# Kernel tuning notes

Measured on AMD Instinct MI355X. Metric: run time of the kernel, lower is better.

Reference implementation:

```python
import jax, jax.numpy as jnp
import numpy as np


def _gcn_conv(x, src, dst, W, b, n_nodes):
    # PyG GCNConv: add self-loops, symmetric deg^{-1/2} normalization, then linear.
    xw = x @ W  # [N, H]
    # degree including self-loop (count of incoming edges at dst + 1)
    deg = jnp.zeros((n_nodes,), dtype=xw.dtype).at[dst].add(1.0) + 1.0
    dinv = jax.lax.rsqrt(deg)  # deg >= 1 always
    coef = (dinv[src] * dinv[dst])[:, None]  # [E, 1]
    out = jnp.zeros_like(xw).at[dst].add(xw[src] * coef)
    # self-loop edge i->i has norm dinv[i]^2
    out = out + xw * (dinv * dinv)[:, None]
    return out + b


def setup_inputs() -> dict:
    key = jax.random.key(0)
    ks = jax.random.split(key, 6)
    N, E, F, H, G = 200000, 600000, 128, 128, 64
    x = jax.random.normal(ks[0], (N, F), dtype=jnp.float32)
    edge_index = jax.random.randint(ks[1], (2, E), 0, N, dtype=jnp.int64)
    batch = jnp.sort(jax.random.randint(ks[2], (N,), 0, G, dtype=jnp.int64))
    W1 = jax.random.normal(ks[3], (F, H), dtype=jnp.float32) * (1.0 / np.sqrt(F))
    b1 = jnp.zeros((H,), dtype=jnp.float32)
    W2 = jax.random.normal(ks[4], (H, H), dtype=jnp.float32) * (1.0 / np.sqrt(H))
    b2 = jnp.zeros((H,), dtype=jnp.float32)
    return {"x": x, "edge_index": edge_index, "batch": batch, "num_graphs": G,
            "W1": W1, "b1": b1, "W2": W2, "b2": b2}


def reference(x, edge_index, batch, num_graphs, W1, b1, W2, b2):
    n_nodes = x.shape[0]
    # feature standardization (torch .std is unbiased, ddof=1)
    x = (x - x.mean(axis=0, keepdims=True)) / x.std(axis=0, keepdims=True, ddof=1)
    src, dst = edge_index[0], edge_index[1]
    h = jax.nn.relu(_gcn_conv(x, src, dst, W1, b1, n_nodes))
    # dropout p=0 -> identity
    h = jax.nn.relu(_gcn_conv(h, src, dst, W2, b2, n_nodes))
    # global_add_pool over batch ids
    return jax.ops.segment_sum(h, batch, num_segments=num_graphs)
```

## Files before the change

### kernel.cpp

```cpp
#include <hip/hip_runtime.h>

#define FDIM 128

typedef __attribute__((ext_vector_type(8))) short short8;
typedef __attribute__((ext_vector_type(4))) float f32x4;

__device__ inline unsigned short f2bf(float f) {
    unsigned int u = __float_as_uint(f);
    unsigned int r = u + 0x7FFFu + ((u >> 16) & 1u);
    return (unsigned short)(r >> 16);
}
__device__ inline float bf2f(unsigned short b) {
    return __uint_as_float((unsigned int)b << 16);
}
__device__ inline void bf8_fma(short8 v, float c, float* acc) {
#pragma unroll
    for (int k = 0; k < 8; ++k)
        acc[k] = fmaf(bf2f(((const unsigned short*)&v)[k]), c, acc[k]);
}

__global__ __launch_bounds__(256) void pre_combo(const float* __restrict__ x, int N,
                                                 float* __restrict__ partials, int statBlocks,
                                                 const int* __restrict__ dst, int E,
                                                 int* __restrict__ cnt,
                                                 unsigned short* __restrict__ xbf) {
    if ((int)blockIdx.x >= statBlocks) {
        int e = (blockIdx.x - statBlocks) * 256 + threadIdx.x;
        if (e < E) atomicAdd(&cnt[dst[e]], 1);
        return;
    }
    const int c4 = threadIdx.x & 31;
    const int rg = threadIdx.x >> 5;
    float4 s = make_float4(0.f, 0.f, 0.f, 0.f);
    float4 q = make_float4(0.f, 0.f, 0.f, 0.f);
    for (long r = (long)blockIdx.x * 8 + rg; r < N; r += (long)statBlocks * 8) {
        float4 v = ((const float4*)x)[r * 32 + c4];
        s.x += v.x; s.y += v.y; s.z += v.z; s.w += v.w;
        q.x += v.x * v.x; q.y += v.y * v.y; q.z += v.z * v.z; q.w += v.w * v.w;
        ushort4 p;
        p.x = f2bf(v.x); p.y = f2bf(v.y); p.z = f2bf(v.z); p.w = f2bf(v.w);
        ((ushort4*)xbf)[r * 32 + c4] = p;
    }
    __shared__ float red[8][32][8];
    float* p = red[rg][c4];
    p[0] = s.x; p[1] = s.y; p[2] = s.z; p[3] = s.w;
    p[4] = q.x; p[5] = q.y; p[6] = q.z; p[7] = q.w;
    __syncthreads();
    if (rg == 0) {
#pragma unroll
        for (int g = 1; g < 8; ++g) {
            const float* o = red[g][c4];
#pragma unroll
            for (int j = 0; j < 8; ++j) red[0][c4][j] += o[j];
        }
        const float* r0 = red[0][c4];
        float* out = &partials[(size_t)blockIdx.x * 256];
        ((float4*)out)[c4] = make_float4(r0[0], r0[1], r0[2], r0[3]);
        ((float4*)(out + 128))[c4] = make_float4(r0[4], r0[5], r0[6], r0[7]);
    }
}

__global__ __launch_bounds__(256) void mid_combo(const int* __restrict__ cnt, int N,
                                                 int* __restrict__ start,
                                                 int* __restrict__ wcur,
                                                 int* __restrict__ counter,
                                                 float* __restrict__ dinv,
                                                 const float* __restrict__ partials,
                                                 int nblk, int offsBlocks,
                                                 const float* __restrict__ W1,
                                                 const float* __restrict__ W2,
                                                 unsigned short* __restrict__ WT1,
                                                 unsigned short* __restrict__ WT2,
                                                 float* __restrict__ bias0) {
    const int tid = threadIdx.x;
    if ((int)blockIdx.x < offsBlocks) {
        __shared__ int sh[256];
        __shared__ int base;
        int i = blockIdx.x * 256 + tid;
        int v = (i < N) ? cnt[i] : 0;
        sh[tid] = v;
        __syncthreads();
        for (int off = 1; off < 256; off <<= 1) {
            int t = (tid >= off) ? sh[tid - off] : 0;
            __syncthreads();
            sh[tid] += t;
            __syncthreads();
        }
        if (tid == 255) base = atomicAdd(counter, sh[255]);
        __syncthreads();
        int excl = base + sh[tid] - v;
        if (i < N) {
            start[i] = excl;
            wcur[i] = excl;
            dinv[i] = rsqrtf((float)v + 1.0f);
        }
        return;
    }
    const int b = blockIdx.x - offsBlocks;
    const int h = tid & 127;
    const int seg = tid >> 7;
    if (b < 8) {
        __shared__ float red[32][32];
        __shared__ float scol[32], mean_sh[16], rstd_sh[16];
        const int rg = tid >> 3;
        const int f = tid & 7;
        const int colbase = (f < 4) ? (b * 16 + f * 4) : (128 + b * 16 + (f - 4) * 4);
        float4 a = make_float4(0.f, 0.f, 0.f, 0.f);
        for (int row = rg; row < nblk; row += 32) {
            float4 v = *(const float4*)&partials[(size_t)row * 256 + colbase];
            a.x += v.x; a.y += v.y; a.z += v.z; a.w += v.w;
        }
        *(float4*)&red[rg][f * 4] = a;
        __syncthreads();
        if (tid < 32) {
            float s = 0.f;
#pragma unroll
            for (int r = 0; r < 32; ++r) s += red[r][tid];
            scol[tid] = s;
        }
        __syncthreads();
        if (tid < 16) {
            float m = scol[tid] / (float)N;
            float var = (scol[16 + tid] - (float)N * m * m) / (float)(N - 1);
            mean_sh[tid] = m;
            rstd_sh[tid] = rsqrtf(var);
        }
        __syncthreads();
        float acc = 0.f;
#pragma unroll
        for (int jj = 0; jj < 8; ++jj) {
            int jl = seg * 8 + jj;
            int j2 = b * 16 + jl;
            float w = W1[j2 * FDIM + h] * rstd_sh[jl];
            WT1[h * FDIM + j2] = f2bf(w);
            acc += mean_sh[jl] * w;
        }
        unsafeAtomicAdd(&bias0[h], -acc);
    } else {
#pragma unroll
        for (int jj = 0; jj < 8; ++jj) {
            int j2 = (b - 8) * 16 + seg * 8 + jj;
            WT2[h * FDIM + j2] = f2bf(W2[j2 * FDIM + h]);
        }
    }
}

__global__ __launch_bounds__(256) void gemm1_fill(const unsigned short* __restrict__ A,
                                                  const unsigned short* __restrict__ WT,
                                                  const float* __restrict__ bias,
                                                  unsigned short* __restrict__ C, int M,
                                                  int gemmBlocks,
                                                  const int* __restrict__ src,
                                                  const int* __restrict__ dst,
                                                  const float* __restrict__ dinv,
                                                  int* __restrict__ wcur,
                                                  int2* __restrict__ edata, int E) {
    const int tid = threadIdx.x;
    if ((int)blockIdx.x >= gemmBlocks) {
        int e = (blockIdx.x - gemmBlocks) * 256 + tid;
        if (e < E) {
            int s = src[e], d = dst[e];
            int pos = atomicAdd(&wcur[d], 1);
            edata[pos] = make_int2(s, __float_as_int(dinv[s] * dinv[d]));
        }
        return;
    }
    constexpr int LDA = 136;
    __shared__ unsigned short Alds[64 * LDA];
    __shared__ unsigned short Wlds[FDIM * LDA];
    const int row0 = blockIdx.x * 64;

    for (int i = tid; i < FDIM * 16; i += 256) {
        int r = i >> 4, g = i & 15;
        *(int4*)&Wlds[r * LDA + g * 8] = *(const int4*)&WT[r * FDIM + g * 8];
    }
    for (int i = tid; i < 64 * 16; i += 256) {
        int r = i >> 4, g = i & 15;
        int row = row0 + r;
        int4 v = make_int4(0, 0, 0, 0);
        if (row < M) v = *(const int4*)&A[(size_t)row * FDIM + g * 8];
        *(int4*)&Alds[r * LDA + g * 8] = v;
    }
    __syncthreads();

    const int lane = tid & 63;
    const int wave = tid >> 6;
    const int m16 = lane & 15;
    const int quad = lane >> 4;

    f32x4 acc[8];
#pragma unroll
    for (int t = 0; t < 8; ++t) acc[t] = (f32x4){0.f, 0.f, 0.f, 0.f};

    const unsigned short* Abase = &Alds[(wave * 16 + m16) * LDA + quad * 8];
    const unsigned short* Wbase = &Wlds[m16 * LDA + quad * 8];
#pragma unroll
    for (int s = 0; s < 4; ++s) {
        short8 a = *(const short8*)&Abase[s * 32];
#pragma unroll
        for (int t = 0; t < 8; ++t) {
            short8 b = *(const short8*)&Wbase[t * 16 * LDA + s * 32];
            acc[t] = __builtin_amdgcn_mfma_f32_16x16x32_bf16(b, a, acc[t], 0, 0, 0);
        }
    }

    const int r = row0 + wave * 16 + m16;
    if (r < M) {
#pragma unroll
        for (int t = 0; t < 8; ++t) {
            ushort4 o;
            o.x = f2bf(acc[t][0] + bias[t * 16 + quad * 4 + 0]);
            o.y = f2bf(acc[t][1] + bias[t * 16 + quad * 4 + 1]);
            o.z = f2bf(acc[t][2] + bias[t * 16 + quad * 4 + 2]);
            o.w = f2bf(acc[t][3] + bias[t * 16 + quad * 4 + 3]);
            *(ushort4*)&C[(size_t)r * FDIM + t * 16 + quad * 4] = o;
        }
    }
}

__global__ __launch_bounds__(256) void agg_gemm2(const unsigned short* __restrict__ xw,
                                                 const float* __restrict__ dinv,
                                                 const int* __restrict__ start,
                                                 const int* __restrict__ cnt,
                                                 const int2* __restrict__ edata,
                                                 const float* __restrict__ bvec,
                                                 const unsigned short* __restrict__ WT2,
                                                 unsigned short* __restrict__ out,
                                                 int N) {
    const int base = blockIdx.x * 16;
    const int node = base + (threadIdx.x >> 4);
    const int l8 = threadIdx.x & 15;
    const bool active = node < N;
    const int nidx = active ? node : (N - 1);

    const int j = start[nidx];
    const int c = active ? cnt[nidx] : 0;
    const int jb = (c > 0) ? j : 0;
    const int cm = (c > 0) ? c - 1 : 0;

    int2 e[8];
#pragma unroll
    for (int k = 0; k < 8; ++k) e[k] = edata[jb + min(k, cm)];

    float dv = dinv[nidx];
    float d2 = dv * dv;
    float4 b0 = ((const float4*)bvec)[l8 * 2];
    float4 b1v = ((const float4*)bvec)[l8 * 2 + 1];
    float acc[8] = {b0.x, b0.y, b0.z, b0.w, b1v.x, b1v.y, b1v.z, b1v.w};
    short8 sv = *(const short8*)&xw[(size_t)nidx * FDIM + l8 * 8];
    bf8_fma(sv, d2, acc);

    short8 u[8];
#pragma unroll
    for (int k = 0; k < 8; ++k)
        u[k] = *(const short8*)&xw[(size_t)e[k].x * FDIM + l8 * 8];

#pragma unroll
    for (int k = 0; k < 8; ++k) {
        float ck = (k < c) ? __int_as_float(e[k].y) : 0.f;
        bf8_fma(u[k], ck, acc);
    }

    for (int k = 8; k < c; ++k) {
        int2 ed = edata[j + k];
        short8 uu = *(const short8*)&xw[(size_t)ed.x * FDIM + l8 * 8];
        bf8_fma(uu, __int_as_float(ed.y), acc);
    }

    constexpr int LDH = 136;
    __shared__ unsigned short hlds[16 * LDH];
    {
        ushort4 o0, o1;
        if (active) {
            o0.x = f2bf(fmaxf(acc[0], 0.f)); o0.y = f2bf(fmaxf(acc[1], 0.f));
            o0.z = f2bf(fmaxf(acc[2], 0.f)); o0.w = f2bf(fmaxf(acc[3], 0.f));
            o1.x = f2bf(fmaxf(acc[4], 0.f)); o1.y = f2bf(fmaxf(acc[5], 0.f));
            o1.z = f2bf(fmaxf(acc[6], 0.f)); o1.w = f2bf(fmaxf(acc[7], 0.f));
        } else {
            o0.x = 0; o0.y = 0; o0.z = 0; o0.w = 0;
            o1.x = 0; o1.y = 0; o1.z = 0; o1.w = 0;
        }
        unsigned short* hp = &hlds[(threadIdx.x >> 4) * LDH + l8 * 8];
        *(ushort4*)hp = o0;
        *(ushort4*)(hp + 4) = o1;
    }
    __syncthreads();

    const int lane = threadIdx.x & 63;
    const int wave = threadIdx.x >> 6;
    const int m16 = lane & 15;
    const int quad = lane >> 4;
    f32x4 c0 = (f32x4){0.f, 0.f, 0.f, 0.f};
    f32x4 c1 = (f32x4){0.f, 0.f, 0.f, 0.f};
    const unsigned short* Abase = &hlds[m16 * LDH + quad * 8];
    const unsigned short* Wg = &WT2[(size_t)(wave * 32 + m16) * FDIM + quad * 8];
#pragma unroll
    for (int s = 0; s < 4; ++s) {
        short8 a = *(const short8*)&Abase[s * 32];
        short8 w0 = *(const short8*)&Wg[s * 32];
        short8 w1 = *(const short8*)&Wg[16 * FDIM + s * 32];
        c0 = __builtin_amdgcn_mfma_f32_16x16x32_bf16(w0, a, c0, 0, 0, 0);
        c1 = __builtin_amdgcn_mfma_f32_16x16x32_bf16(w1, a, c1, 0, 0, 0);
    }
    const int r = base + m16;
    if (r < N) {
        ushort4 o;
        o.x = f2bf(c0[0]); o.y = f2bf(c0[1]); o.z = f2bf(c0[2]); o.w = f2bf(c0[3]);
        *(ushort4*)&out[(size_t)r * FDIM + wave * 32 + quad * 4] = o;
        o.x = f2bf(c1[0]); o.y = f2bf(c1[1]); o.z = f2bf(c1[2]); o.w = f2bf(c1[3]);
        *(ushort4*)&out[(size_t)r * FDIM + wave * 32 + 16 + quad * 4] = o;
    }
}

template <bool POOL>
__global__ __launch_bounds__(256) void aggregate(const unsigned short* __restrict__ xw,
                                                 const float* __restrict__ dinv,
                                                 const int* __restrict__ start,
                                                 const int* __restrict__ cnt,
                                                 const int2* __restrict__ edata,
                                                 const float* __restrict__ bvec,
                                                 unsigned short* __restrict__ out,
                                                 const int* __restrict__ batch,
                                                 float* __restrict__ pool_part,
                                                 int* __restrict__ ptag,
                                                 float* __restrict__ pooled, int N) {
    const int base = blockIdx.x * 16;
    const int node = base + (threadIdx.x >> 4);
    const int l8 = threadIdx.x & 15;
    const bool active = node < N;
    if (!POOL && !active) return;
    const int nidx = active ? node : (N - 1);

    const int j = start[nidx];
    const int c = active ? cnt[nidx] : 0;
    const int jb = (c > 0) ? j : 0;
    const int cm = (c > 0) ? c - 1 : 0;

    int2 e[8];
#pragma unroll
    for (int k = 0; k < 8; ++k) e[k] = edata[jb + min(k, cm)];

    float dv = dinv[nidx];
    float d2 = dv * dv;
    float4 b0 = ((const float4*)bvec)[l8 * 2];
    float4 b1 = ((const float4*)bvec)[l8 * 2 + 1];
    float acc[8] = {b0.x, b0.y, b0.z, b0.w, b1.x, b1.y, b1.z, b1.w};
    short8 sv = *(const short8*)&xw[(size_t)nidx * FDIM + l8 * 8];
    bf8_fma(sv, d2, acc);

    short8 u[8];
#pragma unroll
    for (int k = 0; k < 8; ++k)
        u[k] = *(const short8*)&xw[(size_t)e[k].x * FDIM + l8 * 8];

#pragma unroll
    for (int k = 0; k < 8; ++k) {
        float ck = (k < c) ? __int_as_float(e[k].y) : 0.f;
        bf8_fma(u[k], ck, acc);
    }

    for (int k = 8; k < c; ++k) {
        int2 ed = edata[j + k];
        short8 uu = *(const short8*)&xw[(size_t)ed.x * FDIM + l8 * 8];
        bf8_fma(uu, __int_as_float(ed.y), acc);
    }

    if constexpr (!POOL) {
        short8 o;
#pragma unroll
        for (int k = 0; k < 8; ++k)
            ((unsigned short*)&o)[k] = f2bf(fmaxf(acc[k], 0.f));
        *(short8*)&out[(size_t)node * FDIM + l8 * 8] = o;
    } else {
        float r[8];
#pragma unroll
        for (int k = 0; k < 8; ++k) r[k] = active ? fmaxf(acc[k], 0.f) : 0.f;
        int g0 = batch[base];
        int g1 = batch[min(base + 15, N - 1)];
        if (g0 == g1) {
            __shared__ float red[16][FDIM];
            float* dst = &red[threadIdx.x >> 4][l8 * 8];
            *(float4*)dst = make_float4(r[0], r[1], r[2], r[3]);
            *(float4*)(dst + 4) = make_float4(r[4], r[5], r[6], r[7]);
            __syncthreads();
            if (threadIdx.x < FDIM) {
                float s = 0.f;
#pragma unroll
                for (int i = 0; i < 16; ++i) s += red[i][threadIdx.x];
                pool_part[(size_t)blockIdx.x * FDIM + threadIdx.x] = s;
                if (threadIdx.x == 0) ptag[blockIdx.x] = g0;
            }
        } else {
            if (threadIdx.x == 0) ptag[blockIdx.x] = -1;
            if (active) {
                int g = batch[node];
#pragma unroll
                for (int k = 0; k < 8; ++k)
                    unsafeAtomicAdd(&pooled[g * FDIM + l8 * 8 + k], r[k]);
            }
        }
    }
}

__global__ __launch_bounds__(128) void pool_reduce(const float* __restrict__ pool_part,
                                                   const int* __restrict__ ptag,
                                                   int nslots, float* __restrict__ out) {
    int per = (nslots + gridDim.x - 1) / gridDim.x;
    int s0 = blockIdx.x * per;
    int s1 = min(s0 + per, nslots);
    int t = threadIdx.x;
    float acc = 0.f;
    int cur = -1;
    for (int s = s0; s < s1; ++s) {
        int g = ptag[s];
        if (g < 0) continue;
        if (g != cur) {
            if (cur >= 0) unsafeAtomicAdd(&out[cur * FDIM + t], acc);
            acc = 0.f;
            cur = g;
        }
        acc += pool_part[(size_t)s * FDIM + t];
    }
    if (cur >= 0) unsafeAtomicAdd(&out[cur * FDIM + t], acc);
}

extern "C" void kernel_launch(void* const* d_in, const int* in_sizes, int n_in,
                              void* d_out, int out_size, void* d_ws, size_t ws_size,
                              hipStream_t stream) {
    const float* x = (const float*)d_in[0];
    const int* ei = (const int*)d_in[1];
    const int* batch = (const int*)d_in[2];
    const float* W1 = (const float*)d_in[4];
    const float* b1 = (const float*)d_in[5];
    const float* W2 = (const float*)d_in[6];
    const float* b2 = (const float*)d_in[7];

    const int N = in_sizes[2];
    const int E = in_sizes[1] / 2;
    const int* srcp = ei;
    const int* dstp = ei + E;

    const size_t NF = (size_t)N * FDIM;
    const int aggGrid = (N + 15) / 16;
    unsigned short* bufA = (unsigned short*)d_ws;
    unsigned short* bufB = bufA + NF;
    int* cnt = (int*)(bufB + NF);
    int* counter = cnt + N;
    float* bias0 = (float*)(counter + 4);
    float* dinv = bias0 + FDIM;
    int* start = (int*)(dinv + N);
    int* wcur = start + N;
    unsigned short* WT1 = (unsigned short*)(wcur + N);
    unsigned short* WT2 = WT1 + FDIM * FDIM;
    int2* edata = (int2*)(WT2 + FDIM * FDIM);
    float* pool_part = (float*)(edata + E);
    int* ptag = (int*)(pool_part + (size_t)aggGrid * FDIM);
    float* partials = (float*)edata;
    const int STAT_BLOCKS = 512;

    hipMemsetAsync(cnt, 0, ((size_t)N + 4 + FDIM) * sizeof(int), stream);
    hipMemsetAsync(d_out, 0, (size_t)out_size * sizeof(float), stream);

    const int degBlocks = (E + 255) / 256;
    const int offsBlocks = (N + 255) / 256;
    const int gemmGrid = (N + 63) / 64;

    pre_combo<<<STAT_BLOCKS + degBlocks, 256, 0, stream>>>(x, N, partials, STAT_BLOCKS,
                                                           dstp, E, cnt, bufB);
    mid_combo<<<offsBlocks + 16, 256, 0, stream>>>(cnt, N, start, wcur, counter, dinv,
                                                   partials, STAT_BLOCKS, offsBlocks,
                                                   W1, W2, WT1, WT2, bias0);

    gemm1_fill<<<gemmGrid + degBlocks, 256, 0, stream>>>(bufB, WT1, bias0, bufA, N,
                                                         gemmGrid, srcp, dstp, dinv,
                                                         wcur, edata, E);

    agg_gemm2<<<aggGrid, 256, 0, stream>>>(bufA, dinv, start, cnt, edata, b1, WT2,
                                           bufB, N);

    aggregate<true><<<aggGrid, 256, 0, stream>>>(bufB, dinv, start, cnt, edata, b2,
                                                 nullptr, batch, pool_part, ptag,
                                                 (float*)d_out, N);
    pool_reduce<<<256, 128, 0, stream>>>(pool_part, ptag, aggGrid, (float*)d_out);
}
```

Before: 411.3 us.

## Process two nodes per thread group in aggregation kernels with interleaved gathers

Both aggregation kernels (agg_gemm2 and the pooling aggregation) now handle 32 nodes per block, so each 16-lane group accumulates two nodes. The neighbour loop is replaced by a paired loop that issues four edge-data and four row gathers per iteration across both nodes, aiming for more memory-level parallelism. The GEMM stage reuses the loaded W2 tile for two 16-row tiles, and the pooling reduction covers 32 rows per block. The cost is twice the accumulator registers and a loop bound set by the larger of the two degrees, which adds padded work. The fixed 8-edge prefetch unroll is also dropped.

```diff
diff --git a/kernel.cpp b/kernel.cpp
--- a/kernel.cpp
+++ b/kernel.cpp
@@ -227,62 +227,67 @@
                                                  const unsigned short* __restrict__ WT2,
                                                  unsigned short* __restrict__ out,
                                                  int N) {
-    const int base = blockIdx.x * 16;
-    const int node = base + (threadIdx.x >> 4);
+    const int base = blockIdx.x * 32;
+    const int gid = threadIdx.x >> 4;
     const int l8 = threadIdx.x & 15;
-    const bool active = node < N;
-    const int nidx = active ? node : (N - 1);
-
-    const int j = start[nidx];
-    const int c = active ? cnt[nidx] : 0;
-    const int jb = (c > 0) ? j : 0;
-    const int cm = (c > 0) ? c - 1 : 0;
-
-    int2 e[8];
-#pragma unroll
-    for (int k = 0; k < 8; ++k) e[k] = edata[jb + min(k, cm)];
-
-    float dv = dinv[nidx];
-    float d2 = dv * dv;
+    const int na = base + gid;
+    const int nb = base + 16 + gid;
+    const bool aa = na < N, ab = nb < N;
+    const int ia = aa ? na : (N - 1);
+    const int ib = ab ? nb : (N - 1);
+
+    const int ja = start[ia]; const int ca = aa ? cnt[ia] : 0;
+    const int jb = start[ib]; const int cb = ab ? cnt[ib] : 0;
+    float dva = dinv[ia], dvb = dinv[ib];
     float4 b0 = ((const float4*)bvec)[l8 * 2];
     float4 b1v = ((const float4*)bvec)[l8 * 2 + 1];
-    float acc[8] = {b0.x, b0.y, b0.z, b0.w, b1v.x, b1v.y, b1v.z, b1v.w};
-    short8 sv = *(const short8*)&xw[(size_t)nidx * FDIM + l8 * 8];
-    bf8_fma(sv, d2, acc);
-
-    short8 u[8];
-#pragma unroll
-    for (int k = 0; k < 8; ++k)
-        u[k] = *(const short8*)&xw[(size_t)e[k].x * FDIM + l8 * 8];
-
-#pragma unroll
-    for (int k = 0; k < 8; ++k) {
-        float ck = (k < c) ? __int_as_float(e[k].y) : 0.f;
-        bf8_fma(u[k], ck, acc);
-    }
-
-    for (int k = 8; k < c; ++k) {
-        int2 ed = edata[j + k];
-        short8 uu = *(const short8*)&xw[(size_t)ed.x * FDIM + l8 * 8];
-        bf8_fma(uu, __int_as_float(ed.y), acc);
+    short8 sva = *(const short8*)&xw[(size_t)ia * FDIM + l8 * 8];
+    short8 svb = *(const short8*)&xw[(size_t)ib * FDIM + l8 * 8];
+
+    float accA[8] = {b0.x, b0.y, b0.z, b0.w, b1v.x, b1v.y, b1v.z, b1v.w};
+    float accB[8] = {b0.x, b0.y, b0.z, b0.w, b1v.x, b1v.y, b1v.z, b1v.w};
+    bf8_fma(sva, dva * dva, accA);
+    bf8_fma(svb, dvb * dvb, accB);
+
+    const int jba = (ca > 0) ? ja : 0, cma = (ca > 0) ? ca - 1 : 0;
+    const int jbb = (cb > 0) ? jb : 0, cmb = (cb > 0) ? cb - 1 : 0;
+    const int cmax = max(ca, cb);
+    for (int k = 0; k < cmax; k += 2) {
+        int2 e0a = edata[jba + min(k, cma)];
+        int2 e0b = edata[jbb + min(k, cmb)];
+        int2 e1a = edata[jba + min(k + 1, cma)];
+        int2 e1b = edata[jbb + min(k + 1, cmb)];
+        short8 u0a = *(const short8*)&xw[(size_t)e0a.x * FDIM + l8 * 8];
+        short8 u0b = *(const short8*)&xw[(size_t)e0b.x * FDIM + l8 * 8];
+        short8 u1a = *(const short8*)&xw[(size_t)e1a.x * FDIM + l8 * 8];
+        short8 u1b = *(const short8*)&xw[(size_t)e1b.x * FDIM + l8 * 8];
+        bf8_fma(u0a, (k < ca) ? __int_as_float(e0a.y) : 0.f, accA);
+        bf8_fma(u0b, (k < cb) ? __int_as_float(e0b.y) : 0.f, accB);
+        bf8_fma(u1a, (k + 1 < ca) ? __int_as_float(e1a.y) : 0.f, accA);
+        bf8_fma(u1b, (k + 1 < cb) ? __int_as_float(e1b.y) : 0.f, accB);
     }
 
     constexpr int LDH = 136;
-    __shared__ unsigned short hlds[16 * LDH];
+    __shared__ unsigned short hlds[32 * LDH];
     {
         ushort4 o0, o1;
-        if (active) {
-            o0.x = f2bf(fmaxf(acc[0], 0.f)); o0.y = f2bf(fmaxf(acc[1], 0.f));
-            o0.z = f2bf(fmaxf(acc[2], 0.f)); o0.w = f2bf(fmaxf(acc[3], 0.f));
-            o1.x = f2bf(fmaxf(acc[4], 0.f)); o1.y = f2bf(fmaxf(acc[5], 0.f));
-            o1.z = f2bf(fmaxf(acc[6], 0.f)); o1.w = f2bf(fmaxf(acc[7], 0.f));
-        } else {
-            o0.x = 0; o0.y = 0; o0.z = 0; o0.w = 0;
-            o1.x = 0; o1.y = 0; o1.z = 0; o1.w = 0;
-        }
-        unsigned short* hp = &hlds[(threadIdx.x >> 4) * LDH + l8 * 8];
-        *(ushort4*)hp = o0;
-        *(ushort4*)(hp + 4) = o1;
+#pragma unroll
+        for (int half = 0; half < 2; ++half) {
+            const float* acc = half ? accB : accA;
+            bool act = half ? ab : aa;
+            if (act) {
+                o0.x = f2bf(fmaxf(acc[0], 0.f)); o0.y = f2bf(fmaxf(acc[1], 0.f));
+                o0.z = f2bf(fmaxf(acc[2], 0.f)); o0.w = f2bf(fmaxf(acc[3], 0.f));
+                o1.x = f2bf(fmaxf(acc[4], 0.f)); o1.y = f2bf(fmaxf(acc[5], 0.f));
+                o1.z = f2bf(fmaxf(acc[6], 0.f)); o1.w = f2bf(fmaxf(acc[7], 0.f));
+            } else {
+                o0.x = 0; o0.y = 0; o0.z = 0; o0.w = 0;
+                o1.x = 0; o1.y = 0; o1.z = 0; o1.w = 0;
+            }
+            unsigned short* hp = &hlds[(half * 16 + gid) * LDH + l8 * 8];
+            *(ushort4*)hp = o0;
+            *(ushort4*)(hp + 4) = o1;
+        }
     }
     __syncthreads();
 
@@ -290,114 +295,118 @@
     const int wave = threadIdx.x >> 6;
     const int m16 = lane & 15;
     const int quad = lane >> 4;
-    f32x4 c0 = (f32x4){0.f, 0.f, 0.f, 0.f};
-    f32x4 c1 = (f32x4){0.f, 0.f, 0.f, 0.f};
-    const unsigned short* Abase = &hlds[m16 * LDH + quad * 8];
     const unsigned short* Wg = &WT2[(size_t)(wave * 32 + m16) * FDIM + quad * 8];
 #pragma unroll
-    for (int s = 0; s < 4; ++s) {
-        short8 a = *(const short8*)&Abase[s * 32];
-        short8 w0 = *(const short8*)&Wg[s * 32];
-        short8 w1 = *(const short8*)&Wg[16 * FDIM + s * 32];
-        c0 = __builtin_amdgcn_mfma_f32_16x16x32_bf16(w0, a, c0, 0, 0, 0);
-        c1 = __builtin_amdgcn_mfma_f32_16x16x32_bf16(w1, a, c1, 0, 0, 0);
-    }
-    const int r = base + m16;
-    if (r < N) {
-        ushort4 o;
-        o.x = f2bf(c0[0]); o.y = f2bf(c0[1]); o.z = f2bf(c0[2]); o.w = f2bf(c0[3]);
-        *(ushort4*)&out[(size_t)r * FDIM + wave * 32 + quad * 4] = o;
-        o.x = f2bf(c1[0]); o.y = f2bf(c1[1]); o.z = f2bf(c1[2]); o.w = f2bf(c1[3]);
-        *(ushort4*)&out[(size_t)r * FDIM + wave * 32 + 16 + quad * 4] = o;
-    }
-}
-
-template <bool POOL>
-__global__ __launch_bounds__(256) void aggregate(const unsigned short* __restrict__ xw,
-                                                 const float* __restrict__ dinv,
-                                                 const int* __restrict__ start,
-                                                 const int* __restrict__ cnt,
-                                                 const int2* __restrict__ edata,
-                                                 const float* __restrict__ bvec,
-                                                 unsigned short* __restrict__ out,
-                                                 const int* __restrict__ batch,
-                                                 float* __restrict__ pool_part,
-                                                 int* __restrict__ ptag,
-                                                 float* __restrict__ pooled, int N) {
-    const int base = blockIdx.x * 16;
-    const int node = base + (threadIdx.x >> 4);
+    for (int t = 0; t < 2; ++t) {
+        f32x4 c0 = (f32x4){0.f, 0.f, 0.f, 0.f};
+        f32x4 c1 = (f32x4){0.f, 0.f, 0.f, 0.f};
+        const unsigned short* Abase = &hlds[(t * 16 + m16) * LDH + quad * 8];
+#pragma unroll
+        for (int s = 0; s < 4; ++s) {
+            short8 a = *(const short8*)&Abase[s * 32];
+            short8 w0 = *(const short8*)&Wg[s * 32];
+            short8 w1 = *(const short8*)&Wg[16 * FDIM + s * 32];
+            c0 = __builtin_amdgcn_mfma_f32_16x16x32_bf16(w0, a, c0, 0, 0, 0);
+            c1 = __builtin_amdgcn_mfma_f32_16x16x32_bf16(w1, a, c1, 0, 0, 0);
+        }
+        const int r = base + t * 16 + m16;
+        if (r < N) {
+            ushort4 o;
+            o.x = f2bf(c0[0]); o.y = f2bf(c0[1]); o.z = f2bf(c0[2]); o.w = f2bf(c0[3]);
+            *(ushort4*)&out[(size_t)r * FDIM + wave * 32 + quad * 4] = o;
+            o.x = f2bf(c1[0]); o.y = f2bf(c1[1]); o.z = f2bf(c1[2]); o.w = f2bf(c1[3]);
+            *(ushort4*)&out[(size_t)r * FDIM + wave * 32 + 16 + quad * 4] = o;
+        }
+    }
+}
+
+__global__ __launch_bounds__(256) void agg_pool(const unsigned short* __restrict__ xw,
+                                                const float* __restrict__ dinv,
+                                                const int* __restrict__ start,
+                                                const int* __restrict__ cnt,
+                                                const int2* __restrict__ edata,
+                                                const float* __restrict__ bvec,
+                                                const int* __restrict__ batch,
+                                                float* __restrict__ pool_part,
+                                                int* __restrict__ ptag,
+                                                float* __restrict__ pooled, int N) {
+    const int base = blockIdx.x * 32;
+    const int gid = threadIdx.x >> 4;
     const int l8 = threadIdx.x & 15;
-    const bool active = node < N;
-    if (!POOL && !active) return;
-    const int nidx = active ? node : (N - 1);
-
-    const int j = start[nidx];
-    const int c = active ? cnt[nidx] : 0;
-    const int jb = (c > 0) ? j : 0;
-    const int cm = (c > 0) ? c - 1 : 0;
-
-    int2 e[8];
-#pragma unroll
-    for (int k = 0; k < 8; ++k) e[k] = edata[jb + min(k, cm)];
-
-    float dv = dinv[nidx];
-    float d2 = dv * dv;
+    const int na = base + gid;
+    const int nb = base + 16 + gid;
+    const bool aa = na < N, ab = nb < N;
+    const int ia = aa ? na : (N - 1);
+    const int ib = ab ? nb : (N - 1);
+
+    const int ja = start[ia]; const int ca = aa ? cnt[ia] : 0;
+    const int jb = start[ib]; const int cb = ab ? cnt[ib] : 0;
+    float dva = dinv[ia], dvb = dinv[ib];
     float4 b0 = ((const float4*)bvec)[l8 * 2];
-    float4 b1 = ((const float4*)bvec)[l8 * 2 + 1];
-    float acc[8] = {b0.x, b0.y, b0.z, b0.w, b1.x, b1.y, b1.z, b1.w};
-    short8 sv = *(const short8*)&xw[(size_t)nidx * FDIM + l8 * 8];
-    bf8_fma(sv, d2, acc);
-
-    short8 u[8];
-#pragma unroll
-    for (int k = 0; k < 8; ++k)
-        u[k] = *(const short8*)&xw[(size_t)e[k].x * FDIM + l8 * 8];
-
+    float4 b1v = ((const float4*)bvec)[l8 * 2 + 1];
+    short8 sva = *(const short8*)&xw[(size_t)ia * FDIM + l8 * 8];
+    short8 svb = *(const short8*)&xw[(size_t)ib * FDIM + l8 * 8];
+
+    float accA[8] = {b0.x, b0.y, b0.z, b0.w, b1v.x, b1v.y, b1v.z, b1v.w};
+    float accB[8] = {b0.x, b0.y, b0.z, b0.w, b1v.x, b1v.y, b1v.z, b1v.w};
+    bf8_fma(sva, dva * dva, accA);
+    bf8_fma(svb, dvb * dvb, accB);
+
+    const int jba = (ca > 0) ? ja : 0, cma = (ca > 0) ? ca - 1 : 0;
+    const int jbb = (cb > 0) ? jb : 0, cmb = (cb > 0) ? cb - 1 : 0;
+    const int cmax = max(ca, cb);
+    for (int k = 0; k < cmax; k += 2) {
+        int2 e0a = edata[jba + min(k, cma)];
+        int2 e0b = edata[jbb + min(k, cmb)];
+        int2 e1a = edata[jba + min(k + 1, cma)];
+        int2 e1b = edata[jbb + min(k + 1, cmb)];
+        short8 u0a = *(const short8*)&xw[(size_t)e0a.x * FDIM + l8 * 8];
+        short8 u0b = *(const short8*)&xw[(size_t)e0b.x * FDIM + l8 * 8];
+        short8 u1a = *(const short8*)&xw[(size_t)e1a.x * FDIM + l8 * 8];
+        short8 u1b = *(const short8*)&xw[(size_t)e1b.x * FDIM + l8 * 8];
+        bf8_fma(u0a, (k < ca) ? __int_as_float(e0a.y) : 0.f, accA);
+        bf8_fma(u0b, (k < cb) ? __int_as_float(e0b.y) : 0.f, accB);
+        bf8_fma(u1a, (k + 1 < ca) ? __int_as_float(e1a.y) : 0.f, accA);
+        bf8_fma(u1b, (k + 1 < cb) ? __int_as_float(e1b.y) : 0.f, accB);
+    }
+
+    float rA[8], rB[8];
 #pragma unroll
     for (int k = 0; k < 8; ++k) {
-        float ck = (k < c) ? __int_as_float(e[k].y) : 0.f;
-        bf8_fma(u[k], ck, acc);
-    }
-
-    for (int k = 8; k < c; ++k) {
-        int2 ed = edata[j + k];
-        short8 uu = *(const short8*)&xw[(size_t)ed.x * FDIM + l8 * 8];
-        bf8_fma(uu, __int_as_float(ed.y), acc);
-    }
-
-    if constexpr (!POOL) {
-        short8 o;
-#pragma unroll
-        for (int k = 0; k < 8; ++k)
-            ((unsigned short*)&o)[k] = f2bf(fmaxf(acc[k], 0.f));
-        *(short8*)&out[(size_t)node * FDIM + l8 * 8] = o;
+        rA[k] = aa ? fmaxf(accA[k], 0.f) : 0.f;
+        rB[k] = ab ? fmaxf(accB[k], 0.f) : 0.f;
+    }
+    int g0 = batch[base];
+    int g1 = batch[min(base + 31, N - 1)];
+    if (g0 == g1) {
+        __shared__ float red[32][FDIM];
+        float* dA = &red[gid][l8 * 8];
+        *(float4*)dA = make_float4(rA[0], rA[1], rA[2], rA[3]);
+        *(float4*)(dA + 4) = make_float4(rA[4], rA[5], rA[6], rA[7]);
+        float* dB = &red[16 + gid][l8 * 8];
+        *(float4*)dB = make_float4(rB[0], rB[1], rB[2], rB[3]);
+        *(float4*)(dB + 4) = make_float4(rB[4], rB[5], rB[6], rB[7]);
+        __syncthreads();
+        if (threadIdx.x < FDIM) {
+            float s = 0.f;
+#pragma unroll
+            for (int i = 0; i < 32; ++i) s += red[i][threadIdx.x];
+            pool_part[(size_t)blockIdx.x * FDIM + threadIdx.x] = s;
+            if (threadIdx.x == 0) ptag[blockIdx.x] = g0;
+        }
     } else {
-        float r[8];
-#pragma unroll
-        for (int k = 0; k < 8; ++k) r[k] = active ? fmaxf(acc[k], 0.f) : 0.f;
-        int g0 = batch[base];
-        int g1 = batch[min(base + 15, N - 1)];
-        if (g0 == g1) {
-            __shared__ float red[16][FDIM];
-            float* dst = &red[threadIdx.x >> 4][l8 * 8];
-            *(float4*)dst = make_float4(r[0], r[1], r[2], r[3]);
-            *(float4*)(dst + 4) = make_float4(r[4], r[5], r[6], r[7]);
-            __syncthreads();
-            if (threadIdx.x < FDIM) {
-                float s = 0.f;
-#pragma unroll
-                for (int i = 0; i < 16; ++i) s += red[i][threadIdx.x];
-                pool_part[(size_t)blockIdx.x * FDIM + threadIdx.x] = s;
-                if (threadIdx.x == 0) ptag[blockIdx.x] = g0;
-            }
-        } else {
-            if (threadIdx.x == 0) ptag[blockIdx.x] = -1;
-            if (active) {
-                int g = batch[node];
-#pragma unroll
-                for (int k = 0; k < 8; ++k)
-                    unsafeAtomicAdd(&pooled[g * FDIM + l8 * 8 + k], r[k]);
-            }
+        if (threadIdx.x == 0) ptag[blockIdx.x] = -1;
+        if (aa) {
+            int g = batch[na];
+#pragma unroll
+            for (int k = 0; k < 8; ++k)
+                unsafeAtomicAdd(&pooled[g * FDIM + l8 * 8 + k], rA[k]);
+        }
+        if (ab) {
+            int g = batch[nb];
+#pragma unroll
+            for (int k = 0; k < 8; ++k)
+                unsafeAtomicAdd(&pooled[g * FDIM + l8 * 8 + k], rB[k]);
         }
     }
 }
@@ -441,7 +450,7 @@
     const int* dstp = ei + E;
 
     const size_t NF = (size_t)N * FDIM;
-    const int aggGrid = (N + 15) / 16;
+    const int aggGrid = (N + 31) / 32;
     unsigned short* bufA = (unsigned short*)d_ws;
     unsigned short* bufB = bufA + NF;
     int* cnt = (int*)(bufB + NF);
@@ -478,8 +487,7 @@
     agg_gemm2<<<aggGrid, 256, 0, stream>>>(bufA, dinv, start, cnt, edata, b1, WT2,
                                            bufB, N);
 
-    aggregate<true><<<aggGrid, 256, 0, stream>>>(bufB, dinv, start, cnt, edata, b2,
-                                                 nullptr, batch, pool_part, ptag,
-                                                 (float*)d_out, N);
+    agg_pool<<<aggGrid, 256, 0, stream>>>(bufB, dinv, start, cnt, edata, b2,
+                                          batch, pool_part, ptag, (float*)d_out, N);
     pool_reduce<<<256, 128, 0, stream>>>(pool_part, ptag, aggGrid, (float*)d_out);
 }
```

New measurement: 392.3 us. 1.05x faster.
